# Optimization experiments

Hardware: AMD Instinct MI355X
Metric: run time of the kernel (lower is better)

Reference implementation:

```python
import jax, jax.numpy as jnp
import numpy as np

E = 1024   # embedding_size
H = 16     # num_heads
DH = E // H


def setup_inputs() -> dict:
    key = jax.random.key(0)
    ks = jax.random.split(key, 11)
    B, S = 2, 2048
    std = 0.02
    return {
        "query": jax.random.normal(ks[0], (B, S, E), jnp.float32),
        "key": jax.random.normal(ks[1], (B, S, E), jnp.float32),
        "value": jax.random.normal(ks[2], (B, S, E), jnp.float32),
        "Wq": jax.random.normal(ks[3], (E, E), jnp.float32) * std,
        "bq": jnp.zeros((E,), jnp.float32),
        "Wk": jax.random.normal(ks[4], (E, E), jnp.float32) * std,
        "bk": jnp.zeros((E,), jnp.float32),
        "Wv": jax.random.normal(ks[5], (E, E), jnp.float32) * std,
        "bv": jnp.zeros((E,), jnp.float32),
        "Wo": jax.random.normal(ks[6], (E, E), jnp.float32) * std,
        "bo": jnp.zeros((E,), jnp.float32),
    }


def _split_heads(x, B, S):
    # [B,S,E] -> [B,H,S,DH]
    return x.reshape(B, S, H, DH).transpose(0, 2, 1, 3)


def reference(query, key, value, Wq, bq, Wk, bk, Wv, bv, Wo, bo):
    B, S, _ = query.shape
    # torch Linear: y = x @ W.T + b
    q = _split_heads(query @ Wq.T + bq, B, S)
    k = _split_heads(key @ Wk.T + bk, B, key.shape[1])
    v = _split_heads(value @ Wv.T + bv, B, value.shape[1])
    # naive unscaled attention (original has no 1/sqrt(d) factor)
    scores = jnp.einsum("bhsd,bhtd->bhst", q, k)  # [B,H,S,T]
    attn = jax.nn.softmax(scores, axis=-1)
    out = jnp.einsum("bhst,bhtd->bhsd", attn, v)  # [B,H,S,DH]
    out = out.transpose(0, 2, 1, 3).reshape(B, S, E)
    return out @ Wo.T + bo
```

## Files before the change

kernel.cpp:

```cpp
#include <hip/hip_runtime.h>
#include <hip/hip_bf16.h>

constexpr int kB   = 2;
constexpr int kS   = 2048;
constexpr int kE   = 1024;
constexpr int kH   = 16;
constexpr int kDH  = 64;
constexpr int kTok = kB * kS;

constexpr float kLog2e = 1.4426950408889634f;

typedef short bf16x8 __attribute__((ext_vector_type(8)));
typedef float f32x4  __attribute__((ext_vector_type(4)));
typedef unsigned int uint2v __attribute__((ext_vector_type(2)));

__device__ __forceinline__ float bf2f(unsigned short s) {
  union { unsigned int u; float f; } c; c.u = ((unsigned int)s) << 16; return c.f;
}
__device__ __forceinline__ unsigned short f2bf(float f) {
  union { float f; unsigned int u; } c; c.f = f;
  unsigned int u = c.u;
  u += 0x7fffu + ((u >> 16) & 1u);
  return (unsigned short)(u >> 16);
}

__device__ __forceinline__ unsigned cvtpk(float lo, float hi) {
  unsigned r;
  asm("v_cvt_pk_bf16_f32 %0, %1, %2" : "=v"(r) : "v"(lo), "v"(hi));
  return r;
}

__device__ __forceinline__ float fexp2(float x) {
  float r;
  asm("v_exp_f32 %0, %1" : "=v"(r) : "v"(x));
  return r;
}

__device__ __forceinline__ void gl_lds16(const unsigned short* g, unsigned short* l) {
  __builtin_amdgcn_global_load_lds(
      (const __attribute__((address_space(1))) unsigned int*)g,
      (__attribute__((address_space(3))) unsigned int*)l, 16, 0, 0);
}

__global__ void detect_dtype(const unsigned short* __restrict__ q, int* flag) {
  __shared__ int cnt;
  if (threadIdx.x == 0) cnt = 0;
  __syncthreads();
  int bad = 0;
  for (int i = threadIdx.x; i < 4096; i += 256) {
    unsigned int e = (q[i] >> 7) & 0xFF;
    if (e >= 0xC0) bad++;
  }
  atomicAdd(&cnt, bad);
  __syncthreads();
  if (threadIdx.x == 0) *flag = (cnt > 8) ? 1 : 0;
}

struct Seg { const void* src; unsigned short* dst; unsigned int n; unsigned int blk0; };
struct ConvArgs { Seg s[11]; float scale[11]; };

__global__ __launch_bounds__(256) void conv_all(ConvArgs a, const int* __restrict__ flag) {
  const unsigned int bid = blockIdx.x;
  int si = 0;
  #pragma unroll
  for (int i = 1; i < 11; ++i)
    if (bid >= a.s[i].blk0) si = i;
  const Seg sg = a.s[si];
  const float sc = a.scale[si];
  const int i0 = ((int)(bid - sg.blk0) * 256 + threadIdx.x) * 8;
  if (i0 >= (int)sg.n) return;
  if (*flag) {
    const float* s = (const float*)sg.src + i0;
    f32x4 f0 = *(const f32x4*)(s);
    f32x4 f1 = *(const f32x4*)(s + 4);
    bf16x8 v;
    #pragma unroll
    for (int j = 0; j < 4; ++j) v[j]     = (short)f2bf(f0[j] * sc);
    #pragma unroll
    for (int j = 0; j < 4; ++j) v[j + 4] = (short)f2bf(f1[j] * sc);
    *(bf16x8*)&sg.dst[i0] = v;
  } else {
    bf16x8 v = *(const bf16x8*)((const unsigned short*)sg.src + i0);
    if (sc != 1.0f) {
      #pragma unroll
      for (int j = 0; j < 8; ++j)
        v[j] = (short)f2bf(bf2f((unsigned short)v[j]) * sc);
    }
    *(bf16x8*)&sg.dst[i0] = v;
  }
}

__device__ __forceinline__ void gemm_core(
    const unsigned short* __restrict__ A,
    const unsigned short* __restrict__ W,
    int Kdim, int bM, int bN,
    unsigned short* As, unsigned short* Ws,
    f32x4 acc[4][4])
{
  const int tid  = threadIdx.x;
  const int lane = tid & 63;
  const int wv   = tid >> 6;
  const int wm   = (wv >> 1) * 64;
  const int wn   = (wv & 1) * 64;
  const int lr   = lane & 15;
  const int kq   = (lane >> 4) * 8;

  const int r0 = tid >> 2;
  const int c0 = (tid & 3) * 8;

  const unsigned short* Ag = A + (size_t)(bM + r0) * Kdim + c0;
  const unsigned short* Wg = W + (size_t)(bN + r0) * Kdim + c0;
  unsigned short* lA = &As[tid * 8];
  unsigned short* lW = &Ws[tid * 8];

  gl_lds16(Ag,                      lA);
  gl_lds16(Ag + (size_t)64 * Kdim,  lA + 2048);
  gl_lds16(Wg,                      lW);
  gl_lds16(Wg + (size_t)64 * Kdim,  lW + 2048);
  __syncthreads();

  for (int k0 = 0; k0 < Kdim; k0 += 32) {
    const int co = ((k0 >> 5) & 1) * 4096;
    if (k0 + 32 < Kdim) {
      const int no = co ^ 4096;
      gl_lds16(Ag + k0 + 32,                      lA + no);
      gl_lds16(Ag + (size_t)64 * Kdim + k0 + 32,  lA + no + 2048);
      gl_lds16(Wg + k0 + 32,                      lW + no);
      gl_lds16(Wg + (size_t)64 * Kdim + k0 + 32,  lW + no + 2048);
    }

    bf16x8 a[4], b[4];
    #pragma unroll
    for (int i = 0; i < 4; ++i)
      a[i] = *(const bf16x8*)&As[co + (wm + i * 16 + lr) * 32 + kq];
    #pragma unroll
    for (int i = 0; i < 4; ++i)
      b[i] = *(const bf16x8*)&Ws[co + (wn + i * 16 + lr) * 32 + kq];
    #pragma unroll
    for (int i = 0; i < 4; ++i)
      #pragma unroll
      for (int j = 0; j < 4; ++j)
        acc[i][j] = __builtin_amdgcn_mfma_f32_16x16x32_bf16(a[i], b[j], acc[i][j], 0, 0, 0);

    __syncthreads();
  }
}

__device__ __forceinline__ void gemm_core64(
    const unsigned short* __restrict__ A,
    const unsigned short* __restrict__ W,
    int Kdim, int bM, int bN,
    unsigned short* As, unsigned short* Ws,
    f32x4 acc[4][4])
{
  const int tid  = threadIdx.x;
  const int lane = tid & 63;
  const int wv   = tid >> 6;
  const int wm   = (wv >> 1) * 64;
  const int wn   = (wv & 1) * 64;
  const int lr   = lane & 15;
  const int kq   = (lane >> 4) * 8;

  const int r0 = tid >> 3;
  const int c0 = (tid & 7) * 8;

  const unsigned short* Ag = A + (size_t)(bM + r0) * Kdim + c0;
  const unsigned short* Wg = W + (size_t)(bN + r0) * Kdim + c0;
  unsigned short* lA = &As[tid * 8];
  unsigned short* lW = &Ws[tid * 8];

  #pragma unroll
  for (int j = 0; j < 4; ++j) {
    gl_lds16(Ag + (size_t)(32 * j) * Kdim, lA + j * 2048);
    gl_lds16(Wg + (size_t)(32 * j) * Kdim, lW + j * 2048);
  }
  __syncthreads();

  for (int k0 = 0; k0 < Kdim; k0 += 64) {
    const int co = ((k0 >> 6) & 1) * 8192;
    if (k0 + 64 < Kdim) {
      const int no = co ^ 8192;
      #pragma unroll
      for (int j = 0; j < 4; ++j) {
        gl_lds16(Ag + (size_t)(32 * j) * Kdim + k0 + 64, lA + no + j * 2048);
        gl_lds16(Wg + (size_t)(32 * j) * Kdim + k0 + 64, lW + no + j * 2048);
      }
    }
    #pragma unroll
    for (int kk2 = 0; kk2 < 2; ++kk2) {
      bf16x8 a[4], b[4];
      #pragma unroll
      for (int i = 0; i < 4; ++i)
        a[i] = *(const bf16x8*)&As[co + (wm + i * 16 + lr) * 64 + kk2 * 32 + kq];
      #pragma unroll
      for (int i = 0; i < 4; ++i)
        b[i] = *(const bf16x8*)&Ws[co + (wn + i * 16 + lr) * 64 + kk2 * 32 + kq];
      #pragma unroll
      for (int i = 0; i < 4; ++i)
        #pragma unroll
        for (int j = 0; j < 4; ++j)
          acc[i][j] = __builtin_amdgcn_mfma_f32_16x16x32_bf16(a[i], b[j], acc[i][j], 0, 0, 0);
    }
    __syncthreads();
  }
}

__global__ __launch_bounds__(256) void gemm_qkv(
    const unsigned short* __restrict__ Abase,
    const unsigned short* __restrict__ Wbase,
    const unsigned short* __restrict__ biasbase,
    unsigned short* __restrict__ Cbase)
{
  __shared__ unsigned short As[2 * 128 * 32];
  __shared__ unsigned short Ws[2 * 128 * 32];

  const int bid = blockIdx.x + (blockIdx.y << 3) + (blockIdx.z << 8);
  const int swz = (bid & 7) * 96 + (bid >> 3);
  const int z   = swz >> 8;
  const int rem = swz & 255;
  const int bM  = (rem >> 3) * 128;
  const int bN  = (rem & 7) * 128;

  const unsigned short* A    = Abase    + (size_t)z * (kTok * kE);
  const unsigned short* W    = Wbase    + (size_t)z * (kE * kE);
  const unsigned short* bias = biasbase + (size_t)z * kE;
  unsigned short* C          = Cbase    + (size_t)z * (kTok * kE);

  f32x4 acc[4][4] = {};
  gemm_core(A, W, kE, bM, bN, As, Ws, acc);

  const int lane = threadIdx.x & 63;
  const int wv   = threadIdx.x >> 6;
  const int wm   = (wv >> 1) * 64;
  const int wn   = (wv & 1) * 64;
  const int lr   = lane & 15;
  const int qd   = lane >> 4;
  #pragma unroll
  for (int j = 0; j < 4; ++j) {
    const int col = bN + wn + j * 16 + lr;
    const float bb = bf2f(bias[col]);
    #pragma unroll
    for (int i = 0; i < 4; ++i)
      #pragma unroll
      for (int r = 0; r < 4; ++r) {
        const int row = bM + wm + i * 16 + qd * 4 + r;
        C[(size_t)row * kE + col] = f2bf(acc[i][j][r] + bb);
      }
  }
}

__global__ __launch_bounds__(256) void vtrans(
    const unsigned short* __restrict__ Vb,
    unsigned short* __restrict__ Vt)
{
  __shared__ unsigned short Lt[64 * 72];
  const int tid = threadIdx.x;
  const int bh  = blockIdx.y;
  const int b   = bh >> 4;
  const int h   = bh & 15;
  const int hcol = h * kDH;
  const int s0  = blockIdx.x * 64;

  #pragma unroll
  for (int issue = 0; issue < 2; ++issue) {
    int g = issue * 256 + tid;
    int r = g >> 3, c = (g & 7) * 8;
    bf16x8 vv = *(const bf16x8*)&Vb[(size_t)(b * kS + s0 + r) * kE + hcol + c];
    const int swz = ((((r >> 3) ^ (c >> 3)) & 7) << 3) + (r & 7);
    #pragma unroll
    for (int i = 0; i < 8; ++i)
      Lt[(c + i) * 72 + swz] = (unsigned short)vv[i];
  }
  __syncthreads();
  #pragma unroll
  for (int issue = 0; issue < 2; ++issue) {
    int g = issue * 256 + tid;
    int f = g >> 3, tc = (g & 7) * 8;
    const int blk = ((tc >> 3) ^ (f >> 3)) & 7;
    bf16x8 vv = *(const bf16x8*)&Lt[f * 72 + (blk << 3)];
    *(bf16x8*)&Vt[(size_t)b * (kE * kS) + (size_t)(hcol + f) * kS + s0 + tc] = vv;
  }
}

__global__ __launch_bounds__(256) void gemm_out(
    const unsigned short* __restrict__ A,
    const unsigned short* __restrict__ W,
    const unsigned short* __restrict__ bias,
    void* __restrict__ C,
    const int* __restrict__ flag)
{
  __shared__ unsigned short As[2 * 128 * 64];
  __shared__ unsigned short Ws[2 * 128 * 64];

  const int bid = blockIdx.x + (blockIdx.y << 3);
  const int swz = (bid & 7) * 32 + (bid >> 3);
  const int bM  = (swz >> 3) * 128;
  const int bN  = (swz & 7) * 128;

  f32x4 acc[4][4] = {};
  gemm_core64(A, W, kE, bM, bN, As, Ws, acc);

  const int lane = threadIdx.x & 63;
  const int wv   = threadIdx.x >> 6;
  const int wm   = (wv >> 1) * 64;
  const int wn   = (wv & 1) * 64;
  const int lr   = lane & 15;
  const int qd   = lane >> 4;
  if (*flag) {
    float* Cf = (float*)C;
    #pragma unroll
    for (int j = 0; j < 4; ++j) {
      const int col = bN + wn + j * 16 + lr;
      const float bb = bf2f(bias[col]);
      #pragma unroll
      for (int i = 0; i < 4; ++i)
        #pragma unroll
        for (int r = 0; r < 4; ++r) {
          const int row = bM + wm + i * 16 + qd * 4 + r;
          Cf[(size_t)row * kE + col] = acc[i][j][r] + bb;
        }
    }
  } else {
    unsigned short* Cb = (unsigned short*)C;
    #pragma unroll
    for (int j = 0; j < 4; ++j) {
      const int col = bN + wn + j * 16 + lr;
      const float bb = bf2f(bias[col]);
      #pragma unroll
      for (int i = 0; i < 4; ++i)
        #pragma unroll
        for (int r = 0; r < 4; ++r) {
          const int row = bM + wm + i * 16 + qd * 4 + r;
          Cb[(size_t)row * kE + col] = f2bf(acc[i][j][r] + bb);
        }
    }
  }
}

__global__ __launch_bounds__(256) void attn(
    const unsigned short* __restrict__ Qb,
    const unsigned short* __restrict__ Kb,
    const unsigned short* __restrict__ Vt,
    unsigned short* __restrict__ Ob)
{
  __shared__ unsigned short Ks[2][64 * 72];
  __shared__ unsigned short Vs[2][64 * 72];

  const int tid  = threadIdx.x;
  const int lane = tid & 63;
  const int w    = tid >> 6;
  const int lr   = lane & 15;
  const int quad = lane >> 4;
  const int kq   = quad * 8;

  const int bid = blockIdx.x + (blockIdx.y << 4);
  const int swz = (bid & 7) * 64 + (bid >> 3);
  const int bh  = swz >> 4;
  const int b   = bh >> 4;
  const int h   = bh & 15;
  const int q0  = (swz & 15) * 128;

  const size_t rowbase = (size_t)b * kS * kE;
  const int hcol = h * kDH;
  const unsigned short* Vbase = Vt + (size_t)b * (kE * kS) + (size_t)hcol * kS;

  const int r0 = tid >> 3;
  const int c0 = (tid & 7) * 8;

  bf16x8 aq[2][2];
  #pragma unroll
  for (int rg = 0; rg < 2; ++rg)
    #pragma unroll
    for (int hh = 0; hh < 2; ++hh)
      aq[rg][hh] = *(const bf16x8*)
          &Qb[rowbase + (size_t)(q0 + w * 32 + rg * 16 + lr) * kE + hcol + hh * 32 + kq];

  bf16x8 ones;
  #pragma unroll
  for (int j = 0; j < 8; ++j) ones[j] = (short)0x3F80;

  f32x4 o[2][4] = {};
  f32x4 ol[2]   = {};

  bf16x8 rk0 = *(const bf16x8*)&Kb[rowbase + (size_t)(r0)      * kE + hcol + c0];
  bf16x8 rk1 = *(const bf16x8*)&Kb[rowbase + (size_t)(r0 + 32) * kE + hcol + c0];
  bf16x8 rv0 = *(const bf16x8*)&Vbase[(size_t)(r0)      * kS + c0];
  bf16x8 rv1 = *(const bf16x8*)&Vbase[(size_t)(r0 + 32) * kS + c0];
  *(bf16x8*)&Ks[0][ r0       * 72 + c0] = rk0;
  *(bf16x8*)&Ks[0][(r0 + 32) * 72 + c0] = rk1;
  *(bf16x8*)&Vs[0][ r0       * 72 + c0] = rv0;
  *(bf16x8*)&Vs[0][(r0 + 32) * 72 + c0] = rv1;
  rk0 = *(const bf16x8*)&Kb[rowbase + (size_t)(64 + r0)      * kE + hcol + c0];
  rk1 = *(const bf16x8*)&Kb[rowbase + (size_t)(64 + r0 + 32) * kE + hcol + c0];
  rv0 = *(const bf16x8*)&Vbase[(size_t)(r0)      * kS + 64 + c0];
  rv1 = *(const bf16x8*)&Vbase[(size_t)(r0 + 32) * kS + 64 + c0];
  __syncthreads();

  for (int t0 = 0; t0 < kS; t0 += 64) {
    const int cur = (t0 >> 6) & 1;
    const int nxt = cur ^ 1;

    if (t0 + 64 < kS) {
      *(bf16x8*)&Ks[nxt][ r0       * 72 + c0] = rk0;
      *(bf16x8*)&Ks[nxt][(r0 + 32) * 72 + c0] = rk1;
      *(bf16x8*)&Vs[nxt][ r0       * 72 + c0] = rv0;
      *(bf16x8*)&Vs[nxt][(r0 + 32) * 72 + c0] = rv1;
    }
    if (t0 + 128 < kS) {
      const int t2 = t0 + 128;
      rk0 = *(const bf16x8*)&Kb[rowbase + (size_t)(t2 + r0)      * kE + hcol + c0];
      rk1 = *(const bf16x8*)&Kb[rowbase + (size_t)(t2 + r0 + 32) * kE + hcol + c0];
      rv0 = *(const bf16x8*)&Vbase[(size_t)(r0)      * kS + t2 + c0];
      rv1 = *(const bf16x8*)&Vbase[(size_t)(r0 + 32) * kS + t2 + c0];
    }

    f32x4 s[2][4];
    #pragma unroll
    for (int rg = 0; rg < 2; ++rg)
      #pragma unroll
      for (int tn = 0; tn < 4; ++tn)
        s[rg][tn] = f32x4{0.f, 0.f, 0.f, 0.f};
    __builtin_amdgcn_s_setprio(1);
    #pragma unroll
    for (int tn = 0; tn < 4; ++tn) {
      const bf16x8 bk0 = *(const bf16x8*)&Ks[cur][(tn * 16 + lr) * 72 + 0 + kq];
      const bf16x8 bk1 = *(const bf16x8*)&Ks[cur][(tn * 16 + lr) * 72 + 32 + kq];
      #pragma unroll
      for (int rg = 0; rg < 2; ++rg) {
        s[rg][tn] = __builtin_amdgcn_mfma_f32_16x16x32_bf16(bk0, aq[rg][0], s[rg][tn], 0, 0, 0);
        s[rg][tn] = __builtin_amdgcn_mfma_f32_16x16x32_bf16(bk1, aq[rg][1], s[rg][tn], 0, 0, 0);
      }
    }
    __builtin_amdgcn_s_setprio(0);

    #pragma unroll
    for (int rg = 0; rg < 2; ++rg)
      #pragma unroll
      for (int tn = 0; tn < 4; ++tn)
        #pragma unroll
        for (int r = 0; r < 4; ++r)
          s[rg][tn][r] = fexp2(s[rg][tn][r]);

    bf16x8 ap[2][2];
    #pragma unroll
    for (int rg = 0; rg < 2; ++rg)
      #pragma unroll
      for (int kk = 0; kk < 2; ++kk) {
        const unsigned A0 = cvtpk(s[rg][2 * kk][0],     s[rg][2 * kk][1]);
        const unsigned A1 = cvtpk(s[rg][2 * kk + 1][0], s[rg][2 * kk + 1][1]);
        const uint2v u   = __builtin_amdgcn_permlane32_swap(A0, A1, false, false);
        const uint2v z02 = __builtin_amdgcn_permlane16_swap(u[0], u[1], false, false);
        const unsigned B0 = cvtpk(s[rg][2 * kk][2],     s[rg][2 * kk][3]);
        const unsigned B1 = cvtpk(s[rg][2 * kk + 1][2], s[rg][2 * kk + 1][3]);
        const uint2v v2  = __builtin_amdgcn_permlane32_swap(B0, B1, false, false);
        const uint2v z13 = __builtin_amdgcn_permlane16_swap(v2[0], v2[1], false, false);
        union { unsigned ud[4]; bf16x8 v; } pk;
        pk.ud[0] = z02[0];
        pk.ud[1] = z13[0];
        pk.ud[2] = z02[1];
        pk.ud[3] = z13[1];
        ap[rg][kk] = pk.v;
      }

    __builtin_amdgcn_s_setprio(1);
    #pragma unroll
    for (int kk = 0; kk < 2; ++kk) {
      #pragma unroll
      for (int dt = 0; dt < 4; ++dt) {
        const bf16x8 bv = *(const bf16x8*)&Vs[cur][(dt * 16 + lr) * 72 + kk * 32 + kq];
        #pragma unroll
        for (int rg = 0; rg < 2; ++rg)
          o[rg][dt] = __builtin_amdgcn_mfma_f32_16x16x32_bf16(ap[rg][kk], bv, o[rg][dt], 0, 0, 0);
      }
      #pragma unroll
      for (int rg = 0; rg < 2; ++rg)
        ol[rg] = __builtin_amdgcn_mfma_f32_16x16x32_bf16(ap[rg][kk], ones, ol[rg], 0, 0, 0);
    }
    __builtin_amdgcn_s_setprio(0);

    __syncthreads();
  }

  #pragma unroll
  for (int rg = 0; rg < 2; ++rg) {
    float inv[4];
    #pragma unroll
    for (int r = 0; r < 4; ++r)
      inv[r] = 1.0f / ol[rg][r];

    #pragma unroll
    for (int dt = 0; dt < 4; ++dt) {
      #pragma unroll
      for (int r = 0; r < 4; ++r) {
        const int row = q0 + w * 32 + rg * 16 + quad * 4 + r;
        const int col = hcol + dt * 16 + lr;
        Ob[rowbase + (size_t)row * kE + col] = f2bf(o[rg][dt][r] * inv[r]);
      }
    }
  }
}

extern "C" void kernel_launch(void* const* d_in, const int* in_sizes, int n_in,
                              void* d_out, int out_size, void* d_ws, size_t ws_size,
                              hipStream_t stream) {
  const int nQKV = kTok * kE;
  const int nW   = kE * kE;
  const int nB   = kE;

  char* wsb = (char*)d_ws;
  int* flag = (int*)wsb;
  unsigned short* qc  = (unsigned short*)(wsb + 16);
  unsigned short* kc  = qc  + (size_t)nQKV;
  unsigned short* vc  = kc  + (size_t)nQKV;
  unsigned short* Wqc = vc  + (size_t)nQKV;
  unsigned short* Wkc = Wqc + (size_t)nW;
  unsigned short* Wvc = Wkc + (size_t)nW;
  unsigned short* Woc = Wvc + (size_t)nW;
  unsigned short* bqc = Woc + (size_t)nW;
  unsigned short* bkc = bqc + nB;
  unsigned short* bvc = bkc + nB;
  unsigned short* boc = bvc + nB;
  unsigned short* Qb  = boc + nB;
  unsigned short* Kb  = Qb  + (size_t)nQKV;
  unsigned short* Vb  = Kb  + (size_t)nQKV;
  unsigned short* Vtb = kc;
  unsigned short* Ob  = qc;

  detect_dtype<<<1, 256, 0, stream>>>((const unsigned short*)d_in[0], flag);

  ConvArgs ca;
  const void* srcs[11] = { d_in[0], d_in[1], d_in[2], d_in[3], d_in[4], d_in[5],
                           d_in[6], d_in[7], d_in[8], d_in[9], d_in[10] };
  unsigned short* dsts[11] = { qc, kc, vc, Wqc, bqc, Wkc, bkc, Wvc, bvc, Woc, boc };
  const unsigned int ns[11] = { (unsigned)nQKV, (unsigned)nQKV, (unsigned)nQKV,
                                (unsigned)nW, (unsigned)nB, (unsigned)nW, (unsigned)nB,
                                (unsigned)nW, (unsigned)nB, (unsigned)nW, (unsigned)nB };
  unsigned int blk = 0;
  for (int i = 0; i < 11; ++i) {
    ca.s[i].src = srcs[i]; ca.s[i].dst = dsts[i]; ca.s[i].n = ns[i]; ca.s[i].blk0 = blk;
    ca.scale[i] = 1.0f;
    blk += (ns[i] + 2047) / 2048;
  }
  ca.scale[3] = kLog2e;
  ca.scale[4] = kLog2e;
  conv_all<<<blk, 256, 0, stream>>>(ca, flag);

  dim3 blk256(256);
  dim3 gqkv(kE / 128, kTok / 128, 3);
  gemm_qkv<<<gqkv, blk256, 0, stream>>>(qc, Wqc, bqc, Qb);

  dim3 gvt(kS / 64, kB * kH);
  vtrans<<<gvt, blk256, 0, stream>>>(Vb, Vtb);

  dim3 gattn(kS / 128, kB * kH);
  attn<<<gattn, blk256, 0, stream>>>(Qb, Kb, Vtb, Ob);

  dim3 gout(kE / 128, kTok / 128);
  gemm_out<<<gout, blk256, 0, stream>>>(Ob, Woc, boc, d_out, flag);
}
```

Baseline: 245.9 us.

## Double KV tile to 128 keys and compute softmax row sums in registers

The attention kernel now stages 128-key K/V tiles per iteration instead of 64. This halves the number of barriers and loop iterations and gives longer MFMA runs per tile. The row-sum MFMA against a ones vector is replaced by scalar accumulation of the exponentials in registers, followed by cross-lane shuffles at the end. The trade-off is more LDS (double-buffered tiles roughly double) and more registers for scores and prefetch, which can lower occupancy. The row sum is also now accumulated in fp32 before bf16 rounding, which changes numerics slightly.

```diff
diff --git a/kernel.cpp b/kernel.cpp
--- a/kernel.cpp
+++ b/kernel.cpp
@@ -343,8 +343,8 @@
     const unsigned short* __restrict__ Vt,
     unsigned short* __restrict__ Ob)
 {
-  __shared__ unsigned short Ks[2][64 * 72];
-  __shared__ unsigned short Vs[2][64 * 72];
+  __shared__ unsigned short Ks[2][128 * 72];
+  __shared__ unsigned short Vs[2][64 * 136];
 
   const int tid  = threadIdx.x;
   const int lane = tid & 63;
@@ -364,8 +364,10 @@
   const int hcol = h * kDH;
   const unsigned short* Vbase = Vt + (size_t)b * (kE * kS) + (size_t)hcol * kS;
 
-  const int r0 = tid >> 3;
-  const int c0 = (tid & 7) * 8;
+  const int kr = tid >> 3;
+  const int kc = (tid & 7) * 8;
+  const int vr = tid >> 2;
+  const int vc = (tid & 3) * 8;
 
   bf16x8 aq[2][2];
   #pragma unroll
@@ -375,54 +377,56 @@
       aq[rg][hh] = *(const bf16x8*)
           &Qb[rowbase + (size_t)(q0 + w * 32 + rg * 16 + lr) * kE + hcol + hh * 32 + kq];
 
-  bf16x8 ones;
-  #pragma unroll
-  for (int j = 0; j < 8; ++j) ones[j] = (short)0x3F80;
-
   f32x4 o[2][4] = {};
-  f32x4 ol[2]   = {};
-
-  bf16x8 rk0 = *(const bf16x8*)&Kb[rowbase + (size_t)(r0)      * kE + hcol + c0];
-  bf16x8 rk1 = *(const bf16x8*)&Kb[rowbase + (size_t)(r0 + 32) * kE + hcol + c0];
-  bf16x8 rv0 = *(const bf16x8*)&Vbase[(size_t)(r0)      * kS + c0];
-  bf16x8 rv1 = *(const bf16x8*)&Vbase[(size_t)(r0 + 32) * kS + c0];
-  *(bf16x8*)&Ks[0][ r0       * 72 + c0] = rk0;
-  *(bf16x8*)&Ks[0][(r0 + 32) * 72 + c0] = rk1;
-  *(bf16x8*)&Vs[0][ r0       * 72 + c0] = rv0;
-  *(bf16x8*)&Vs[0][(r0 + 32) * 72 + c0] = rv1;
-  rk0 = *(const bf16x8*)&Kb[rowbase + (size_t)(64 + r0)      * kE + hcol + c0];
-  rk1 = *(const bf16x8*)&Kb[rowbase + (size_t)(64 + r0 + 32) * kE + hcol + c0];
-  rv0 = *(const bf16x8*)&Vbase[(size_t)(r0)      * kS + 64 + c0];
-  rv1 = *(const bf16x8*)&Vbase[(size_t)(r0 + 32) * kS + 64 + c0];
+  float l4[2][4] = {};
+
+  bf16x8 rk[4], rv[4];
+  #pragma unroll
+  for (int j = 0; j < 4; ++j) {
+    rk[j] = *(const bf16x8*)&Kb[rowbase + (size_t)(kr + 32 * j) * kE + hcol + kc];
+    rv[j] = *(const bf16x8*)&Vbase[(size_t)vr * kS + vc + 32 * j];
+  }
+  #pragma unroll
+  for (int j = 0; j < 4; ++j) {
+    *(bf16x8*)&Ks[0][(kr + 32 * j) * 72 + kc] = rk[j];
+    *(bf16x8*)&Vs[0][vr * 136 + vc + 32 * j]  = rv[j];
+  }
+  #pragma unroll
+  for (int j = 0; j < 4; ++j) {
+    rk[j] = *(const bf16x8*)&Kb[rowbase + (size_t)(128 + kr + 32 * j) * kE + hcol + kc];
+    rv[j] = *(const bf16x8*)&Vbase[(size_t)vr * kS + 128 + vc + 32 * j];
+  }
   __syncthreads();
 
-  for (int t0 = 0; t0 < kS; t0 += 64) {
-    const int cur = (t0 >> 6) & 1;
+  for (int t0 = 0; t0 < kS; t0 += 128) {
+    const int cur = (t0 >> 7) & 1;
     const int nxt = cur ^ 1;
 
-    if (t0 + 64 < kS) {
-      *(bf16x8*)&Ks[nxt][ r0       * 72 + c0] = rk0;
-      *(bf16x8*)&Ks[nxt][(r0 + 32) * 72 + c0] = rk1;
-      *(bf16x8*)&Vs[nxt][ r0       * 72 + c0] = rv0;
-      *(bf16x8*)&Vs[nxt][(r0 + 32) * 72 + c0] = rv1;
-    }
     if (t0 + 128 < kS) {
-      const int t2 = t0 + 128;
-      rk0 = *(const bf16x8*)&Kb[rowbase + (size_t)(t2 + r0)      * kE + hcol + c0];
-      rk1 = *(const bf16x8*)&Kb[rowbase + (size_t)(t2 + r0 + 32) * kE + hcol + c0];
-      rv0 = *(const bf16x8*)&Vbase[(size_t)(r0)      * kS + t2 + c0];
-      rv1 = *(const bf16x8*)&Vbase[(size_t)(r0 + 32) * kS + t2 + c0];
-    }
-
-    f32x4 s[2][4];
+      #pragma unroll
+      for (int j = 0; j < 4; ++j) {
+        *(bf16x8*)&Ks[nxt][(kr + 32 * j) * 72 + kc] = rk[j];
+        *(bf16x8*)&Vs[nxt][vr * 136 + vc + 32 * j]  = rv[j];
+      }
+    }
+    if (t0 + 256 < kS) {
+      const int t2 = t0 + 256;
+      #pragma unroll
+      for (int j = 0; j < 4; ++j) {
+        rk[j] = *(const bf16x8*)&Kb[rowbase + (size_t)(t2 + kr + 32 * j) * kE + hcol + kc];
+        rv[j] = *(const bf16x8*)&Vbase[(size_t)vr * kS + t2 + vc + 32 * j];
+      }
+    }
+
+    f32x4 s[2][8];
     #pragma unroll
     for (int rg = 0; rg < 2; ++rg)
       #pragma unroll
-      for (int tn = 0; tn < 4; ++tn)
+      for (int tn = 0; tn < 8; ++tn)
         s[rg][tn] = f32x4{0.f, 0.f, 0.f, 0.f};
     __builtin_amdgcn_s_setprio(1);
     #pragma unroll
-    for (int tn = 0; tn < 4; ++tn) {
+    for (int tn = 0; tn < 8; ++tn) {
       const bf16x8 bk0 = *(const bf16x8*)&Ks[cur][(tn * 16 + lr) * 72 + 0 + kq];
       const bf16x8 bk1 = *(const bf16x8*)&Ks[cur][(tn * 16 + lr) * 72 + 32 + kq];
       #pragma unroll
@@ -436,16 +440,19 @@
     #pragma unroll
     for (int rg = 0; rg < 2; ++rg)
       #pragma unroll
-      for (int tn = 0; tn < 4; ++tn)
+      for (int tn = 0; tn < 8; ++tn)
         #pragma unroll
-        for (int r = 0; r < 4; ++r)
-          s[rg][tn][r] = fexp2(s[rg][tn][r]);
-
-    bf16x8 ap[2][2];
+        for (int r = 0; r < 4; ++r) {
+          const float e = fexp2(s[rg][tn][r]);
+          s[rg][tn][r] = e;
+          l4[rg][r] += e;
+        }
+
+    bf16x8 ap[2][4];
     #pragma unroll
     for (int rg = 0; rg < 2; ++rg)
       #pragma unroll
-      for (int kk = 0; kk < 2; ++kk) {
+      for (int kk = 0; kk < 4; ++kk) {
         const unsigned A0 = cvtpk(s[rg][2 * kk][0],     s[rg][2 * kk][1]);
         const unsigned A1 = cvtpk(s[rg][2 * kk + 1][0], s[rg][2 * kk + 1][1]);
         const uint2v u   = __builtin_amdgcn_permlane32_swap(A0, A1, false, false);
@@ -464,18 +471,14 @@
 
     __builtin_amdgcn_s_setprio(1);
     #pragma unroll
-    for (int kk = 0; kk < 2; ++kk) {
+    for (int kk = 0; kk < 4; ++kk)
       #pragma unroll
       for (int dt = 0; dt < 4; ++dt) {
-        const bf16x8 bv = *(const bf16x8*)&Vs[cur][(dt * 16 + lr) * 72 + kk * 32 + kq];
+        const bf16x8 bv = *(const bf16x8*)&Vs[cur][(dt * 16 + lr) * 136 + kk * 32 + kq];
         #pragma unroll
         for (int rg = 0; rg < 2; ++rg)
           o[rg][dt] = __builtin_amdgcn_mfma_f32_16x16x32_bf16(ap[rg][kk], bv, o[rg][dt], 0, 0, 0);
       }
-      #pragma unroll
-      for (int rg = 0; rg < 2; ++rg)
-        ol[rg] = __builtin_amdgcn_mfma_f32_16x16x32_bf16(ap[rg][kk], ones, ol[rg], 0, 0, 0);
-    }
     __builtin_amdgcn_s_setprio(0);
 
     __syncthreads();
@@ -483,10 +486,13 @@
 
   #pragma unroll
   for (int rg = 0; rg < 2; ++rg) {
+    float l = (l4[rg][0] + l4[rg][1]) + (l4[rg][2] + l4[rg][3]);
+    l += __shfl_xor(l, 16, 64);
+    l += __shfl_xor(l, 32, 64);
     float inv[4];
     #pragma unroll
     for (int r = 0; r < 4; ++r)
-      inv[r] = 1.0f / ol[rg][r];
+      inv[r] = 1.0f / __shfl(l, quad * 4 + r, 64);
 
     #pragma unroll
     for (int dt = 0; dt < 4; ++dt) {
```

New measurement: 244.7 us. No clear change (-0.5%).
